# Optimization experiments

Measured on AMD Instinct MI355X. Metric: run time of the kernel, lower is better.

Reference implementation:

```python
import jax, jax.numpy as jnp
import numpy as np


@jax.custom_vjp
def binarize_ste(x):
    return jnp.sign(x)


def _binarize_fwd(x):
    return jnp.sign(x), None


def _binarize_bwd(_, g):
    # straight-through estimator: pass gradient through, clamped to [-1, 1]
    return (jnp.clip(g, -1.0, 1.0),)


binarize_ste.defvjp(_binarize_fwd, _binarize_bwd)


def setup_inputs() -> dict:
    key = jax.random.key(0)
    kx, kw = jax.random.split(key)
    x = jax.random.normal(kx, (32, 128, 64, 64), dtype=jnp.float32)  # NCHW
    weight = jax.random.normal(kw, (256, 128, 3, 3), dtype=jnp.float32)  # OIHW
    return {"x": x, "weight": weight}


def reference(x, weight):
    w_bin = binarize_ste(weight)  # +/-1 (0 where weight==0, matching torch.sign)
    out = jax.lax.conv_general_dilated(
        x, w_bin,
        window_strides=(1, 1),
        padding=((1, 1), (1, 1)),
        dimension_numbers=("NCHW", "OIHW", "NCHW"),
    )
    return out
```

## Files before the change

kernel.cpp:

```cpp
#include <hip/hip_runtime.h>
#include <hip/hip_bf16.h>


typedef short bf16x8 __attribute__((ext_vector_type(8)));
typedef float f32x4 __attribute__((ext_vector_type(4)));

#define XT_ELEMS (32 * 66 * 66 * 128)
#define XT_BYTES (XT_ELEMS * 2)

__device__ __forceinline__ void glds16(const void* g, const void* l) {
    __builtin_amdgcn_global_load_lds(
        (const __attribute__((address_space(1))) void*)g,
        (__attribute__((address_space(3))) void*)l, 16, 0, 0);
}

__global__ void prep_w_kernel(const float* __restrict__ w,
                              __hip_bfloat16* __restrict__ wm) {
    int tid = blockIdx.x * 256 + threadIdx.x;
    int o = tid / 1152;
    int r = tid - o * 1152;
    int j = r >> 7;
    int c = r & 127;
    float v = w[o * 1152 + c * 9 + j];
    float s = (v > 0.f) ? 1.f : ((v < 0.f) ? -1.f : 0.f);
    wm[tid] = __float2bfloat16(s);
}

__global__ void transpose_x_kernel(const float* __restrict__ x,
                                   __hip_bfloat16* __restrict__ xt) {
    int n = blockIdx.x >> 6;
    int h = blockIdx.x & 63;
    const float* xp = x + (size_t)n * 524288 + h * 64;
    __hip_bfloat16* xo = xt + ((size_t)(n * 66 + h + 1) * 66 + 1) * 128;
    for (int i = threadIdx.x; i < 8192; i += 256) {
        int w = i >> 7;
        int c = i & 127;
        xo[w * 128 + c] = __float2bfloat16(xp[c * 4096 + w]);
    }
}

__global__ __launch_bounds__(256, 2) void gemm_kernel(
    const __hip_bfloat16* __restrict__ xt,
    const __hip_bfloat16* __restrict__ wm,
    float* __restrict__ out) {
    __shared__ short As[128 * 64];
    __shared__ short Bs[128 * 64];

    const int t = threadIdx.x;
    const int lane = t & 63;
    const int wv = t >> 6;
    const int px_blk = blockIdx.x;
    const int o_blk = blockIdx.y;
    const int n = (px_blk * 128) >> 12;
    const int h0 = ((px_blk * 128) & 4095) >> 6;

    const int wo = (wv & 1) * 64;
    const int wp = (wv >> 1) * 64;
    const int l15 = lane & 15;
    const int quad = lane >> 4;
    const int srow = lane >> 3;
    const int sseg = lane & 7;

    const short* wmS = (const short*)wm + (o_blk * 128) * 1152;
    const short* xtS = (const short*)xt;

    f32x4 acc[4][4] = {};

    for (int j = 0; j < 9; ++j) {
        const int kh = j / 3;
        const int kw = j - kh * 3;
        for (int cc = 0; cc < 128; cc += 64) {
#pragma unroll
            for (int i = 0; i < 4; ++i) {
                const int r0 = wv * 32 + i * 8;
                const int r = r0 + srow;
                const int segl = sseg ^ (r & 7);
                glds16(wmS + r * 1152 + j * 128 + cc + segl * 8,
                       As + r0 * 64);
            }
#pragma unroll
            for (int i = 0; i < 4; ++i) {
                const int r0 = wv * 32 + i * 8;
                const int p = r0 + srow;
                const int hh = h0 + (p >> 6) + kh;
                const int ww = (p & 63) + kw;
                const int segl = sseg ^ (p & 7);
                glds16(xtS + ((size_t)(n * 66 + hh) * 66 + ww) * 128 + cc + segl * 8,
                       Bs + r0 * 64);
            }
            __syncthreads();
#pragma unroll
            for (int kf = 0; kf < 2; ++kf) {
                bf16x8 a[4], b[4];
#pragma unroll
                for (int i = 0; i < 4; ++i) {
                    const int o = wo + i * 16 + l15;
                    const int seg = (kf * 4 + quad) ^ (o & 7);
                    a[i] = *(const bf16x8*)(As + o * 64 + seg * 8);
                }
#pragma unroll
                for (int i = 0; i < 4; ++i) {
                    const int p = wp + i * 16 + l15;
                    const int seg = (kf * 4 + quad) ^ (p & 7);
                    b[i] = *(const bf16x8*)(Bs + p * 64 + seg * 8);
                }
#pragma unroll
                for (int i = 0; i < 4; ++i)
#pragma unroll
                    for (int jj = 0; jj < 4; ++jj)
                        acc[i][jj] = __builtin_amdgcn_mfma_f32_16x16x32_bf16(
                            a[i], b[jj], acc[i][jj], 0, 0, 0);
            }
            __syncthreads();
        }
    }

    const int Pbase = px_blk * 128 + wp;
#pragma unroll
    for (int i = 0; i < 4; ++i) {
#pragma unroll
        for (int jj = 0; jj < 4; ++jj) {
            const int P = Pbase + jj * 16 + l15;
            const int hw = P & 4095;
            float* op = out + (size_t)n * 1048576 + hw;
#pragma unroll
            for (int r = 0; r < 4; ++r) {
                const int o = o_blk * 128 + wo + i * 16 + quad * 4 + r;
                op[(size_t)o * 4096] = acc[i][jj][r];
            }
        }
    }
}

extern "C" void kernel_launch(void* const* d_in, const int* in_sizes, int n_in,
                              void* d_out, int out_size, void* d_ws, size_t ws_size,
                              hipStream_t stream) {
    const float* x = (const float*)d_in[0];
    const float* w = (const float*)d_in[1];
    float* out = (float*)d_out;
    __hip_bfloat16* xt = (__hip_bfloat16*)d_ws;
    __hip_bfloat16* wm = (__hip_bfloat16*)((char*)d_ws + XT_BYTES);

    hipMemsetAsync(d_ws, 0, XT_BYTES, stream);
    prep_w_kernel<<<1152, 256, 0, stream>>>(w, wm);
    transpose_x_kernel<<<2048, 256, 0, stream>>>(x, xt);
    gemm_kernel<<<dim3(1024, 2), 256, 0, stream>>>(xt, wm, out);
}
```

Before: 279.6 us.

## Stage input row-window once per kh and reuse across kw shifts; drop memset

The GEMM tile now covers 256 pixels (4 output rows) per block. For each (cc, kh) it loads a 4x66-cell window of input channels into LDS once and reuses it for all three kw taps by shifting the cell index, instead of reloading a shifted B tile for every tap. The transpose kernel now goes through an LDS tile to write coalesced 32-bit stores and zeroes the padding border itself, which removes the full-buffer memset. In exchange each block holds 8x4 accumulator tiles, which raises register pressure and may lower occupancy under the 2-blocks launch bound.

```diff
diff --git a/kernel.cpp b/kernel.cpp
--- a/kernel.cpp
+++ b/kernel.cpp
@@ -28,14 +28,29 @@
 
 __global__ void transpose_x_kernel(const float* __restrict__ x,
                                    __hip_bfloat16* __restrict__ xt) {
-    int n = blockIdx.x >> 6;
-    int h = blockIdx.x & 63;
+    __shared__ short tl[64 * 130];
+    const int t = threadIdx.x;
+    const int n = blockIdx.x >> 6;
+    const int h = blockIdx.x & 63;
     const float* xp = x + (size_t)n * 524288 + h * 64;
-    __hip_bfloat16* xo = xt + ((size_t)(n * 66 + h + 1) * 66 + 1) * 128;
-    for (int i = threadIdx.x; i < 8192; i += 256) {
-        int w = i >> 7;
-        int c = i & 127;
-        xo[w * 128 + c] = __float2bfloat16(xp[c * 4096 + w]);
+    for (int i = t; i < 8192; i += 256) {
+        int w = i & 63, c = i >> 6;
+        tl[w * 130 + c] = (short)__bfloat16_as_ushort(__float2bfloat16(xp[c * 4096 + w]));
+    }
+    uint* xtn = (uint*)(xt + (size_t)n * 66 * 66 * 128);
+    {
+        int row = h + 1;
+        if (t < 64)       xtn[(row * 66 + 0) * 64 + t] = 0u;
+        else if (t < 128) xtn[(row * 66 + 65) * 64 + (t - 64)] = 0u;
+    }
+    if (h == 0)  for (int i = t; i < 66 * 64; i += 256) xtn[i] = 0u;
+    if (h == 63) for (int i = t; i < 66 * 64; i += 256) xtn[65 * 66 * 64 + i] = 0u;
+    __syncthreads();
+    uint* xo = (uint*)(xt + ((size_t)(n * 66 + h + 1) * 66 + 1) * 128);
+    for (int i = t; i < 4096; i += 256) {
+        int c2 = i & 63;
+        int w = i >> 6;
+        xo[w * 64 + c2] = *(const uint*)(tl + w * 130 + c2 * 2);
     }
 }
 
@@ -44,18 +59,19 @@
     const __hip_bfloat16* __restrict__ wm,
     float* __restrict__ out) {
     __shared__ short As[128 * 64];
-    __shared__ short Bs[128 * 64];
+    __shared__ short Bw[2112 * 8];
 
     const int t = threadIdx.x;
     const int lane = t & 63;
     const int wv = t >> 6;
     const int px_blk = blockIdx.x;
     const int o_blk = blockIdx.y;
-    const int n = (px_blk * 128) >> 12;
-    const int h0 = ((px_blk * 128) & 4095) >> 6;
+    const int n = px_blk >> 4;
+    const int h0 = (px_blk & 15) * 4;
 
     const int wo = (wv & 1) * 64;
-    const int wp = (wv >> 1) * 64;
+    const int wp = (wv >> 1) * 128;
+    const int wpr = wp >> 6;
     const int l15 = lane & 15;
     const int quad = lane >> 4;
     const int srow = lane >> 3;
@@ -64,62 +80,65 @@
     const short* wmS = (const short*)wm + (o_blk * 128) * 1152;
     const short* xtS = (const short*)xt;
 
-    f32x4 acc[4][4] = {};
+    f32x4 acc[4][8] = {};
 
-    for (int j = 0; j < 9; ++j) {
-        const int kh = j / 3;
-        const int kw = j - kh * 3;
-        for (int cc = 0; cc < 128; cc += 64) {
+    for (int cc = 0; cc < 128; cc += 64) {
+        for (int kh = 0; kh < 3; ++kh) {
+            const short* xw = xtS + ((size_t)(n * 66 + h0 + kh) * 66) * 128;
 #pragma unroll
-            for (int i = 0; i < 4; ++i) {
-                const int r0 = wv * 32 + i * 8;
-                const int r = r0 + srow;
-                const int segl = sseg ^ (r & 7);
-                glds16(wmS + r * 1152 + j * 128 + cc + segl * 8,
-                       As + r0 * 64);
+            for (int i = 0; i < 9; ++i) {
+                int bidx = i * 4 + wv;
+                if (bidx < 33) {
+                    int l = bidx * 64 + lane;
+                    int cell = l >> 3;
+                    int q = l & 7;
+                    int s = q ^ (cell & 7);
+                    glds16(xw + cell * 128 + cc + s * 8, Bw + bidx * 512);
+                }
             }
-#pragma unroll
-            for (int i = 0; i < 4; ++i) {
-                const int r0 = wv * 32 + i * 8;
-                const int p = r0 + srow;
-                const int hh = h0 + (p >> 6) + kh;
-                const int ww = (p & 63) + kw;
-                const int segl = sseg ^ (p & 7);
-                glds16(xtS + ((size_t)(n * 66 + hh) * 66 + ww) * 128 + cc + segl * 8,
-                       Bs + r0 * 64);
-            }
-            __syncthreads();
-#pragma unroll
-            for (int kf = 0; kf < 2; ++kf) {
-                bf16x8 a[4], b[4];
+            for (int kw = 0; kw < 3; ++kw) {
+                const int j = kh * 3 + kw;
 #pragma unroll
                 for (int i = 0; i < 4; ++i) {
-                    const int o = wo + i * 16 + l15;
-                    const int seg = (kf * 4 + quad) ^ (o & 7);
-                    a[i] = *(const bf16x8*)(As + o * 64 + seg * 8);
+                    int r0 = wv * 32 + i * 8;
+                    int r = r0 + srow;
+                    int segl = sseg ^ (r & 7);
+                    glds16(wmS + r * 1152 + j * 128 + cc + segl * 8,
+                           As + r0 * 64);
                 }
+                __syncthreads();
 #pragma unroll
-                for (int i = 0; i < 4; ++i) {
-                    const int p = wp + i * 16 + l15;
-                    const int seg = (kf * 4 + quad) ^ (p & 7);
-                    b[i] = *(const bf16x8*)(Bs + p * 64 + seg * 8);
+                for (int kf = 0; kf < 2; ++kf) {
+                    bf16x8 a[4], b[8];
+#pragma unroll
+                    for (int i = 0; i < 4; ++i) {
+                        int o = wo + i * 16 + l15;
+                        int seg = (kf * 4 + quad) ^ (o & 7);
+                        a[i] = *(const bf16x8*)(As + o * 64 + seg * 8);
+                    }
+#pragma unroll
+                    for (int i = 0; i < 8; ++i) {
+                        int cell = (wpr + (i >> 2)) * 66 + (i & 3) * 16 + l15 + kw;
+                        int seg = (kf * 4 + quad) ^ (cell & 7);
+                        b[i] = *(const bf16x8*)(Bw + cell * 64 + seg * 8);
+                    }
+#pragma unroll
+                    for (int i = 0; i < 4; ++i)
+#pragma unroll
+                        for (int jj = 0; jj < 8; ++jj)
+                            acc[i][jj] = __builtin_amdgcn_mfma_f32_16x16x32_bf16(
+                                a[i], b[jj], acc[i][jj], 0, 0, 0);
                 }
-#pragma unroll
-                for (int i = 0; i < 4; ++i)
-#pragma unroll
-                    for (int jj = 0; jj < 4; ++jj)
-                        acc[i][jj] = __builtin_amdgcn_mfma_f32_16x16x32_bf16(
-                            a[i], b[jj], acc[i][jj], 0, 0, 0);
+                __syncthreads();
             }
-            __syncthreads();
         }
     }
 
-    const int Pbase = px_blk * 128 + wp;
+    const int Pbase = px_blk * 256 + wp;
 #pragma unroll
     for (int i = 0; i < 4; ++i) {
 #pragma unroll
-        for (int jj = 0; jj < 4; ++jj) {
+        for (int jj = 0; jj < 8; ++jj) {
             const int P = Pbase + jj * 16 + l15;
             const int hw = P & 4095;
             float* op = out + (size_t)n * 1048576 + hw;
@@ -141,8 +160,7 @@
     __hip_bfloat16* xt = (__hip_bfloat16*)d_ws;
     __hip_bfloat16* wm = (__hip_bfloat16*)((char*)d_ws + XT_BYTES);
 
-    hipMemsetAsync(d_ws, 0, XT_BYTES, stream);
     prep_w_kernel<<<1152, 256, 0, stream>>>(w, wm);
     transpose_x_kernel<<<2048, 256, 0, stream>>>(x, xt);
-    gemm_kernel<<<dim3(1024, 2), 256, 0, stream>>>(xt, wm, out);
+    gemm_kernel<<<dim3(512, 2), 256, 0, stream>>>(xt, wm, out);
 }
```

Result: faster. 248.4 us (-11.2%).
